# Kernel optimization log

Measured on AMD Instinct MI355X. Metric: run time of the kernel, lower is better.

Reference implementation:

```python
import jax, jax.numpy as jnp
import numpy as np

FEATURE_DIM = 768
LAMBDA_REG = 0.01
NUM_ITERS = 5
LR = 0.1
SIGMA = 2.0
MARGIN = 1.0
BN_EPS = 1e-5


def setup_inputs() -> dict:
    key = jax.random.key(0)
    ks = jax.random.split(key, 10)
    B, D = 32, FEATURE_DIM
    search_features = jax.random.normal(ks[0], (B, D, 32, 32), dtype=jnp.float32)
    target_features = jax.random.normal(ks[1], (B, D, 16, 16), dtype=jnp.float32)
    target_mask = jax.random.uniform(ks[2], (B, 1, 16, 16), dtype=jnp.float32)
    conv_w = jax.random.normal(ks[3], (D, D), dtype=jnp.float32) * (1.0 / np.sqrt(D))
    conv_b = jax.random.normal(ks[4], (D,), dtype=jnp.float32) * 0.01
    bn_gamma = jnp.ones((D,), dtype=jnp.float32)
    bn_beta = jnp.zeros((D,), dtype=jnp.float32)
    bn_mean = jax.random.normal(ks[5], (D,), dtype=jnp.float32) * 0.01
    bn_var = jax.random.uniform(ks[6], (D,), dtype=jnp.float32, minval=0.5, maxval=1.5)
    filter_init = jax.random.normal(ks[7], (1, D, 1, 1), dtype=jnp.float32) * 0.01
    return {
        "search_features": search_features,
        "target_features": target_features,
        "target_mask": target_mask,
        "conv_w": conv_w,
        "conv_b": conv_b,
        "bn_gamma": bn_gamma,
        "bn_beta": bn_beta,
        "bn_mean": bn_mean,
        "bn_var": bn_var,
        "filter_init": filter_init,
    }


def _proj(x, conv_w, conv_b, bn_gamma, bn_beta, bn_mean, bn_var):
    # 1x1 conv == channel-wise GEMM, then BatchNorm (eval mode, running stats)
    y = jnp.einsum('bdhw,ed->behw', x, conv_w) + conv_b[None, :, None, None]
    inv_std = bn_gamma / jnp.sqrt(bn_var + BN_EPS)
    return (y - bn_mean[None, :, None, None]) * inv_std[None, :, None, None] + bn_beta[None, :, None, None]


def _gaussian_label(mask):
    B, _, H, W = mask.shape
    yy, xx = jnp.meshgrid(jnp.arange(H, dtype=jnp.float32), jnp.arange(W, dtype=jnp.float32), indexing='ij')
    yy = yy[None, None]  # (1,1,H,W)
    xx = xx[None, None]
    msum = jnp.clip(mask.sum(axis=(2, 3), keepdims=True), 1.0)
    cy = (mask * yy).sum(axis=(2, 3), keepdims=True) / msum
    cx = (mask * xx).sum(axis=(2, 3), keepdims=True) / msum
    return jnp.exp(-((xx - cx) ** 2 + (yy - cy) ** 2) / (2.0 * SIGMA ** 2))


def reference(search_features, target_features, target_mask, conv_w, conv_b,
              bn_gamma, bn_beta, bn_mean, bn_var, filter_init):
    sp = _proj(search_features, conv_w, conv_b, bn_gamma, bn_beta, bn_mean, bn_var)
    tp = _proj(target_features, conv_w, conv_b, bn_gamma, bn_beta, bn_mean, bn_var)
    B = tp.shape[0]
    label = _gaussian_label(target_mask)  # (B,1,H',W')
    f = jnp.broadcast_to(filter_init, (B,) + filter_init.shape[1:])  # (B,D,1,1)
    for _ in range(NUM_ITERS):
        response = (tp * f).sum(axis=1, keepdims=True)  # (B,1,H',W')
        loss = jnp.maximum(MARGIN - response * label, 0.0)
        grad = jnp.where(loss > 0, -label * target_mask, 0.0)
        grad = grad.mean(axis=(2, 3), keepdims=True)  # (B,1,1,1), broadcasts over D
        f = f - LR * (grad + LAMBDA_REG * f)
    return (sp * f).sum(axis=1, keepdims=True)  # (B,1,H,W)
```

## Files before the change

### kernel.cpp

```cpp
#include <hip/hip_runtime.h>
#include <math.h>

#define DD   768
#define BB   32
#define NTP  256
#define NSP  1024
#define NT   (BB*NTP)
#define NS   (BB*NSP)
#define NCH  16
#define CHD  (DD/NCH)
#define ECH  24
#define CHE  (DD/ECH)

#define OFF_UP 0
#define OFF_VP (OFF_UP + ECH*DD)
#define OFF_K  (OFF_VP + ECH*DD)
#define OFF_TR (OFF_K + 16)
#define OFF_TS (OFF_TR + NCH*NT)
#define OFF_SR (OFF_TS + NCH*NT)
#define OFF_SS (OFF_SR + NCH*NS)

__global__ void k_prep(const float* __restrict__ w, const float* __restrict__ cb,
                       const float* __restrict__ gamma, const float* __restrict__ beta,
                       const float* __restrict__ mean, const float* __restrict__ var,
                       const float* __restrict__ fi, float* __restrict__ ws) {
    int bx = blockIdx.x;
    if (bx < 3 * ECH) {
        int db = bx % 3;
        int ec = bx / 3;
        int d = db * 256 + threadIdx.x;
        __shared__ float wu[CHE], wv[CHE];
        if (threadIdx.x < CHE) {
            int e = ec * CHE + threadIdx.x;
            float inv = gamma[e] / sqrtf(var[e] + 1e-5f);
            wv[threadIdx.x] = inv;
            wu[threadIdx.x] = inv * fi[e];
        }
        __syncthreads();
        float au = 0.f, av = 0.f;
        #pragma unroll 8
        for (int j = 0; j < CHE; ++j) {
            float wval = w[(size_t)(ec * CHE + j) * DD + d];
            au += wval * wu[j];
            av += wval * wv[j];
        }
        ws[OFF_UP + ec * DD + d] = au;
        ws[OFF_VP + ec * DD + d] = av;
    } else {
        __shared__ float r1[256], r2[256];
        float a1 = 0.f, a2 = 0.f;
        for (int e = threadIdx.x; e < DD; e += 256) {
            float inv = gamma[e] / sqrtf(var[e] + 1e-5f);
            float t = (cb[e] - mean[e]) * inv + beta[e];
            a1 += t * fi[e];
            a2 += t;
        }
        r1[threadIdx.x] = a1; r2[threadIdx.x] = a2;
        __syncthreads();
        for (int s = 128; s > 0; s >>= 1) {
            if (threadIdx.x < s) { r1[threadIdx.x] += r1[threadIdx.x + s]; r2[threadIdx.x] += r2[threadIdx.x + s]; }
            __syncthreads();
        }
        if (threadIdx.x == 0) { ws[OFF_K] = r1[0]; ws[OFF_K + 1] = r2[0]; }
    }
}

__global__ void k_dots(const float* __restrict__ tf, const float* __restrict__ sf,
                       float* __restrict__ ws) {
    int bx = blockIdx.x;
    int k = bx / 40;
    int r = bx % 40;
    int d0 = k * CHD;
    __shared__ float su[CHD], sv[CHD];
    if (threadIdx.x < CHD) {
        float au = 0.f, av = 0.f;
        #pragma unroll
        for (int ec = 0; ec < ECH; ++ec) {
            au += ws[OFF_UP + ec * DD + d0 + threadIdx.x];
            av += ws[OFF_VP + ec * DD + d0 + threadIdx.x];
        }
        su[threadIdx.x] = au; sv[threadIdx.x] = av;
    }
    __syncthreads();

    const float4* bp;
    int strideF4;
    float4* outR;
    float4* outS;
    if (r < 8) {
        int g = r * 1024 + threadIdx.x * 4;
        int b = g >> 8, p = g & 255;
        bp = (const float4*)(tf + ((size_t)b * DD + d0) * NTP + p);
        strideF4 = NTP / 4;
        outR = (float4*)(ws + OFF_TR + k * NT + g);
        outS = (float4*)(ws + OFF_TS + k * NT + g);
    } else {
        int g = (r - 8) * 1024 + threadIdx.x * 4;
        int b = g >> 10, p = g & 1023;
        bp = (const float4*)(sf + ((size_t)b * DD + d0) * NSP + p);
        strideF4 = NSP / 4;
        outR = (float4*)(ws + OFF_SR + k * NS + g);
        outS = (float4*)(ws + OFF_SS + k * NS + g);
    }
    float arx = 0.f, ary = 0.f, arz = 0.f, arw = 0.f;
    float asx = 0.f, asy = 0.f, asz = 0.f, asw = 0.f;
    #pragma unroll 8
    for (int j = 0; j < CHD; ++j) {
        float4 v = bp[(size_t)j * strideF4];
        float u = su[j], vv = sv[j];
        arx += v.x * u;  ary += v.y * u;  arz += v.z * u;  arw += v.w * u;
        asx += v.x * vv; asy += v.y * vv; asz += v.z * vv; asw += v.w * vv;
    }
    float4 R; R.x = arx; R.y = ary; R.z = arz; R.w = arw;
    float4 S; S.x = asx; S.y = asy; S.z = asz; S.w = asw;
    *outR = R;
    *outS = S;
}

__global__ void k_out(const float* __restrict__ mask, const float* __restrict__ ws,
                      float* __restrict__ out) {
    int b = blockIdx.x;
    int p = threadIdx.x;
    int h = p >> 4, w = p & 15;
    float K1 = ws[OFF_K], K2 = ws[OFF_K + 1];
    float r0 = K1, s0 = K2;
    #pragma unroll
    for (int k = 0; k < NCH; ++k) {
        r0 += ws[OFF_TR + k * NT + b * 256 + p];
        s0 += ws[OFF_TS + k * NT + b * 256 + p];
    }
    float m = mask[b * 256 + p];
    __shared__ float red[256];
    auto block_sum = [&](float v) -> float {
        red[p] = v; __syncthreads();
        for (int s = 128; s > 0; s >>= 1) {
            if (p < s) red[p] += red[p + s];
            __syncthreads();
        }
        float o = red[0]; __syncthreads();
        return o;
    };
    float msum = block_sum(m);
    float sy = block_sum(m * (float)h);
    float sx = block_sum(m * (float)w);
    msum = fmaxf(msum, 1.0f);
    float cy = sy / msum, cx = sx / msum;
    float dx = (float)w - cx, dy = (float)h - cy;
    float label = expf(-(dx * dx + dy * dy) * 0.125f);
    float A = 1.0f, c = 0.0f;
    const float decay = 1.0f - 0.1f * 0.01f;
    #pragma unroll
    for (int it = 0; it < 5; ++it) {
        float resp = A * r0 + c * s0;
        float gc = (1.0f - resp * label > 0.0f) ? (-label * m) : 0.0f;
        float g = block_sum(gc) * (1.0f / 256.0f);
        c = decay * c - 0.1f * g;
        A *= decay;
    }
    int g = b * 1024 + p * 4;
    float rx = K1, ry = K1, rz = K1, rw = K1;
    float sxx = K2, syy = K2, szz = K2, sww = K2;
    #pragma unroll
    for (int k = 0; k < NCH; ++k) {
        float4 tR = *(const float4*)(ws + OFF_SR + k * NS + g);
        float4 tS = *(const float4*)(ws + OFF_SS + k * NS + g);
        rx += tR.x; ry += tR.y; rz += tR.z; rw += tR.w;
        sxx += tS.x; syy += tS.y; szz += tS.z; sww += tS.w;
    }
    const float A5 = 0.99500999000499900f;
    float4 o;
    o.x = A5 * rx + c * sxx;
    o.y = A5 * ry + c * syy;
    o.z = A5 * rz + c * szz;
    o.w = A5 * rw + c * sww;
    *(float4*)(out + g) = o;
}

extern "C" void kernel_launch(void* const* d_in, const int* in_sizes, int n_in,
                              void* d_out, int out_size, void* d_ws, size_t ws_size,
                              hipStream_t stream) {
    const float* sf    = (const float*)d_in[0];
    const float* tf    = (const float*)d_in[1];
    const float* mask  = (const float*)d_in[2];
    const float* w     = (const float*)d_in[3];
    const float* cb    = (const float*)d_in[4];
    const float* gamma = (const float*)d_in[5];
    const float* beta  = (const float*)d_in[6];
    const float* mean  = (const float*)d_in[7];
    const float* var   = (const float*)d_in[8];
    const float* fi    = (const float*)d_in[9];
    float* out = (float*)d_out;
    float* ws  = (float*)d_ws;

    k_prep<<<3 * ECH + 1, 256, 0, stream>>>(w, cb, gamma, beta, mean, var, fi, ws);
    k_dots<<<NCH * 40,    256, 0, stream>>>(tf, sf, ws);
    k_out <<<BB,          256, 0, stream>>>(mask, ws, out);
}
```

Measured before the change: 39.18 us.

## Restructure projection-dot pipeline with fewer channel chunks and in-block wave reduction

Reduces the channel split of the dot kernel from 16 to 2 chunks and splits each 384-channel chunk across four waves, combining their partials through shared memory. The per-block folding of projected weights moves into a new small k_prep2 kernel. k_prep now uses float4 loads over 48 row chunks, and k_out's block reductions use wave shuffles. This cuts workspace partial traffic and redundant per-block weight summing, at the cost of an extra kernel launch and a different grid shape (320 blocks).

```diff
diff --git a/kernel.cpp b/kernel.cpp
--- a/kernel.cpp
+++ b/kernel.cpp
@@ -7,14 +7,16 @@
 #define NSP  1024
 #define NT   (BB*NTP)
 #define NS   (BB*NSP)
-#define NCH  16
+#define NCH  2
 #define CHD  (DD/NCH)
-#define ECH  24
+#define ECH  48
 #define CHE  (DD/ECH)
 
 #define OFF_UP 0
 #define OFF_VP (OFF_UP + ECH*DD)
-#define OFF_K  (OFF_VP + ECH*DD)
+#define OFF_U  (OFF_VP + ECH*DD)
+#define OFF_V  (OFF_U + DD)
+#define OFF_K  (OFF_V + DD)
 #define OFF_TR (OFF_K + 16)
 #define OFF_TS (OFF_TR + NCH*NT)
 #define OFF_SR (OFF_TS + NCH*NT)
@@ -25,124 +27,138 @@
                        const float* __restrict__ mean, const float* __restrict__ var,
                        const float* __restrict__ fi, float* __restrict__ ws) {
     int bx = blockIdx.x;
-    if (bx < 3 * ECH) {
-        int db = bx % 3;
-        int ec = bx / 3;
-        int d = db * 256 + threadIdx.x;
+    int t = threadIdx.x;
+    if (bx < ECH) {
         __shared__ float wu[CHE], wv[CHE];
-        if (threadIdx.x < CHE) {
-            int e = ec * CHE + threadIdx.x;
+        if (t < CHE) {
+            int e = bx * CHE + t;
             float inv = gamma[e] / sqrtf(var[e] + 1e-5f);
-            wv[threadIdx.x] = inv;
-            wu[threadIdx.x] = inv * fi[e];
-        }
-        __syncthreads();
-        float au = 0.f, av = 0.f;
-        #pragma unroll 8
-        for (int j = 0; j < CHE; ++j) {
-            float wval = w[(size_t)(ec * CHE + j) * DD + d];
-            au += wval * wu[j];
-            av += wval * wv[j];
-        }
-        ws[OFF_UP + ec * DD + d] = au;
-        ws[OFF_VP + ec * DD + d] = av;
+            wv[t] = inv;
+            wu[t] = inv * fi[e];
+        }
+        __syncthreads();
+        if (t < 192) {
+            const float4* w4 = (const float4*)w;
+            float4 Ru = {0,0,0,0}, Rv = {0,0,0,0};
+            #pragma unroll
+            for (int j = 0; j < CHE; ++j) {
+                float4 x = w4[(size_t)(bx * CHE + j) * 192 + t];
+                float a = wu[j], b = wv[j];
+                Ru.x += x.x * a; Ru.y += x.y * a; Ru.z += x.z * a; Ru.w += x.w * a;
+                Rv.x += x.x * b; Rv.y += x.y * b; Rv.z += x.z * b; Rv.w += x.w * b;
+            }
+            *(float4*)(ws + OFF_UP + bx * DD + t * 4) = Ru;
+            *(float4*)(ws + OFF_VP + bx * DD + t * 4) = Rv;
+        }
     } else {
         __shared__ float r1[256], r2[256];
         float a1 = 0.f, a2 = 0.f;
-        for (int e = threadIdx.x; e < DD; e += 256) {
+        for (int e = t; e < DD; e += 256) {
             float inv = gamma[e] / sqrtf(var[e] + 1e-5f);
-            float t = (cb[e] - mean[e]) * inv + beta[e];
-            a1 += t * fi[e];
-            a2 += t;
-        }
-        r1[threadIdx.x] = a1; r2[threadIdx.x] = a2;
+            float x = (cb[e] - mean[e]) * inv + beta[e];
+            a1 += x * fi[e];
+            a2 += x;
+        }
+        r1[t] = a1; r2[t] = a2;
         __syncthreads();
         for (int s = 128; s > 0; s >>= 1) {
-            if (threadIdx.x < s) { r1[threadIdx.x] += r1[threadIdx.x + s]; r2[threadIdx.x] += r2[threadIdx.x + s]; }
+            if (t < s) { r1[t] += r1[t + s]; r2[t] += r2[t + s]; }
             __syncthreads();
         }
-        if (threadIdx.x == 0) { ws[OFF_K] = r1[0]; ws[OFF_K + 1] = r2[0]; }
-    }
+        if (t == 0) { ws[OFF_K] = r1[0]; ws[OFF_K + 1] = r2[0]; }
+    }
+}
+
+__global__ void k_prep2(float* __restrict__ ws) {
+    int bx = blockIdx.x;
+    int d = (bx % 3) * 256 + threadIdx.x;
+    int isV = bx / 3;
+    int srcOff = isV ? OFF_VP : OFF_UP;
+    int dstOff = isV ? OFF_V : OFF_U;
+    float a = 0.f;
+    #pragma unroll 8
+    for (int ec = 0; ec < ECH; ++ec) a += ws[srcOff + ec * DD + d];
+    ws[dstOff + d] = a;
 }
 
 __global__ void k_dots(const float* __restrict__ tf, const float* __restrict__ sf,
                        float* __restrict__ ws) {
     int bx = blockIdx.x;
-    int k = bx / 40;
-    int r = bx % 40;
-    int d0 = k * CHD;
+    int lane = threadIdx.x & 63, wv = threadIdx.x >> 6;
     __shared__ float su[CHD], sv[CHD];
-    if (threadIdx.x < CHD) {
-        float au = 0.f, av = 0.f;
-        #pragma unroll
-        for (int ec = 0; ec < ECH; ++ec) {
-            au += ws[OFF_UP + ec * DD + d0 + threadIdx.x];
-            av += ws[OFF_VP + ec * DD + d0 + threadIdx.x];
-        }
-        su[threadIdx.x] = au; sv[threadIdx.x] = av;
+    int cc, grp; bool isT;
+    if (bx < 256) { isT = false; cc = bx & 1; grp = bx >> 1; }
+    else          { isT = true;  int u = bx - 256; cc = u & 1; grp = u >> 1; }
+    int c0 = cc * CHD;
+    for (int d = threadIdx.x; d < CHD; d += 256) {
+        su[d] = ws[OFF_U + c0 + d];
+        sv[d] = ws[OFF_V + c0 + d];
     }
     __syncthreads();
 
     const float4* bp;
     int strideF4;
-    float4* outR;
-    float4* outS;
-    if (r < 8) {
-        int g = r * 1024 + threadIdx.x * 4;
-        int b = g >> 8, p = g & 255;
-        bp = (const float4*)(tf + ((size_t)b * DD + d0) * NTP + p);
+    float4 *outR, *outS;
+    if (!isT) {
+        int b = grp >> 2, q = grp & 3;
+        bp = (const float4*)(sf + ((size_t)b * DD + c0) * NSP + q * 256 + lane * 4);
+        strideF4 = NSP / 4;
+        outR = (float4*)(ws + OFF_SR + cc * NS + grp * 256 + lane * 4);
+        outS = (float4*)(ws + OFF_SS + cc * NS + grp * 256 + lane * 4);
+    } else {
+        bp = (const float4*)(tf + ((size_t)grp * DD + c0) * NTP + lane * 4);
         strideF4 = NTP / 4;
-        outR = (float4*)(ws + OFF_TR + k * NT + g);
-        outS = (float4*)(ws + OFF_TS + k * NT + g);
-    } else {
-        int g = (r - 8) * 1024 + threadIdx.x * 4;
-        int b = g >> 10, p = g & 1023;
-        bp = (const float4*)(sf + ((size_t)b * DD + d0) * NSP + p);
-        strideF4 = NSP / 4;
-        outR = (float4*)(ws + OFF_SR + k * NS + g);
-        outS = (float4*)(ws + OFF_SS + k * NS + g);
-    }
-    float arx = 0.f, ary = 0.f, arz = 0.f, arw = 0.f;
-    float asx = 0.f, asy = 0.f, asz = 0.f, asw = 0.f;
+        outR = (float4*)(ws + OFF_TR + cc * NT + grp * 256 + lane * 4);
+        outS = (float4*)(ws + OFF_TS + cc * NT + grp * 256 + lane * 4);
+    }
+    int jbase = wv * 96;
+    float4 R = {0,0,0,0}, S = {0,0,0,0};
     #pragma unroll 8
-    for (int j = 0; j < CHD; ++j) {
+    for (int k = 0; k < 96; ++k) {
+        int j = jbase + k;
         float4 v = bp[(size_t)j * strideF4];
-        float u = su[j], vv = sv[j];
-        arx += v.x * u;  ary += v.y * u;  arz += v.z * u;  arw += v.w * u;
-        asx += v.x * vv; asy += v.y * vv; asz += v.z * vv; asw += v.w * vv;
-    }
-    float4 R; R.x = arx; R.y = ary; R.z = arz; R.w = arw;
-    float4 S; S.x = asx; S.y = asy; S.z = asz; S.w = asw;
-    *outR = R;
-    *outS = S;
+        float u = su[j], vb = sv[j];
+        R.x += v.x * u;  R.y += v.y * u;  R.z += v.z * u;  R.w += v.w * u;
+        S.x += v.x * vb; S.y += v.y * vb; S.z += v.z * vb; S.w += v.w * vb;
+    }
+    __shared__ float4 redR[4][64], redS[4][64];
+    redR[wv][lane] = R; redS[wv][lane] = S;
+    __syncthreads();
+    if (wv == 0) {
+        float4 r = redR[0][lane], s = redS[0][lane];
+        #pragma unroll
+        for (int u = 1; u < 4; ++u) {
+            float4 a = redR[u][lane], b = redS[u][lane];
+            r.x += a.x; r.y += a.y; r.z += a.z; r.w += a.w;
+            s.x += b.x; s.y += b.y; s.z += b.z; s.w += b.w;
+        }
+        *outR = r; *outS = s;
+    }
 }
 
 __global__ void k_out(const float* __restrict__ mask, const float* __restrict__ ws,
                       float* __restrict__ out) {
     int b = blockIdx.x;
     int p = threadIdx.x;
+    int lane = p & 63, wv = p >> 6;
     int h = p >> 4, w = p & 15;
     float K1 = ws[OFF_K], K2 = ws[OFF_K + 1];
-    float r0 = K1, s0 = K2;
-    #pragma unroll
-    for (int k = 0; k < NCH; ++k) {
-        r0 += ws[OFF_TR + k * NT + b * 256 + p];
-        s0 += ws[OFF_TS + k * NT + b * 256 + p];
-    }
+    float r0 = K1 + ws[OFF_TR + b * 256 + p] + ws[OFF_TR + NT + b * 256 + p];
+    float s0 = K2 + ws[OFF_TS + b * 256 + p] + ws[OFF_TS + NT + b * 256 + p];
     float m = mask[b * 256 + p];
-    __shared__ float red[256];
-    auto block_sum = [&](float v) -> float {
-        red[p] = v; __syncthreads();
-        for (int s = 128; s > 0; s >>= 1) {
-            if (p < s) red[p] += red[p + s];
-            __syncthreads();
-        }
-        float o = red[0]; __syncthreads();
-        return o;
+    __shared__ float cross[4];
+    auto bsum = [&](float v) -> float {
+        #pragma unroll
+        for (int o = 32; o > 0; o >>= 1) v += __shfl_xor(v, o, 64);
+        if (lane == 0) cross[wv] = v;
+        __syncthreads();
+        float r = cross[0] + cross[1] + cross[2] + cross[3];
+        __syncthreads();
+        return r;
     };
-    float msum = block_sum(m);
-    float sy = block_sum(m * (float)h);
-    float sx = block_sum(m * (float)w);
+    float msum = bsum(m);
+    float sy = bsum(m * (float)h);
+    float sx = bsum(m * (float)w);
     msum = fmaxf(msum, 1.0f);
     float cy = sy / msum, cx = sx / msum;
     float dx = (float)w - cx, dy = (float)h - cy;
@@ -153,26 +169,21 @@
     for (int it = 0; it < 5; ++it) {
         float resp = A * r0 + c * s0;
         float gc = (1.0f - resp * label > 0.0f) ? (-label * m) : 0.0f;
-        float g = block_sum(gc) * (1.0f / 256.0f);
+        float g = bsum(gc) * (1.0f / 256.0f);
         c = decay * c - 0.1f * g;
         A *= decay;
     }
     int g = b * 1024 + p * 4;
-    float rx = K1, ry = K1, rz = K1, rw = K1;
-    float sxx = K2, syy = K2, szz = K2, sww = K2;
-    #pragma unroll
-    for (int k = 0; k < NCH; ++k) {
-        float4 tR = *(const float4*)(ws + OFF_SR + k * NS + g);
-        float4 tS = *(const float4*)(ws + OFF_SS + k * NS + g);
-        rx += tR.x; ry += tR.y; rz += tR.z; rw += tR.w;
-        sxx += tS.x; syy += tS.y; szz += tS.z; sww += tS.w;
-    }
+    float4 r1 = *(const float4*)(ws + OFF_SR + g);
+    float4 r2 = *(const float4*)(ws + OFF_SR + NS + g);
+    float4 s1 = *(const float4*)(ws + OFF_SS + g);
+    float4 s2 = *(const float4*)(ws + OFF_SS + NS + g);
     const float A5 = 0.99500999000499900f;
     float4 o;
-    o.x = A5 * rx + c * sxx;
-    o.y = A5 * ry + c * syy;
-    o.z = A5 * rz + c * szz;
-    o.w = A5 * rw + c * sww;
+    o.x = A5 * (K1 + r1.x + r2.x) + c * (K2 + s1.x + s2.x);
+    o.y = A5 * (K1 + r1.y + r2.y) + c * (K2 + s1.y + s2.y);
+    o.z = A5 * (K1 + r1.z + r2.z) + c * (K2 + s1.z + s2.z);
+    o.w = A5 * (K1 + r1.w + r2.w) + c * (K2 + s1.w + s2.w);
     *(float4*)(out + g) = o;
 }
 
@@ -192,7 +203,8 @@
     float* out = (float*)d_out;
     float* ws  = (float*)d_ws;
 
-    k_prep<<<3 * ECH + 1, 256, 0, stream>>>(w, cb, gamma, beta, mean, var, fi, ws);
-    k_dots<<<NCH * 40,    256, 0, stream>>>(tf, sf, ws);
-    k_out <<<BB,          256, 0, stream>>>(mask, ws, out);
-}
+    k_prep <<<ECH + 1, 256, 0, stream>>>(w, cb, gamma, beta, mean, var, fi, ws);
+    k_prep2<<<6,       256, 0, stream>>>(ws);
+    k_dots <<<320,     256, 0, stream>>>(tf, sf, ws);
+    k_out  <<<BB,      256, 0, stream>>>(mask, ws, out);
+}
```

Measured after the change: 50.16 us. 1.28x slower.
